# Optimization experiments

Measured on AMD Instinct MI355X. Metric: run time of the kernel, lower is better.

Reference implementation:

```python
import jax, jax.numpy as jnp
import numpy as np


def _maxpool2(x):
    # 2x2 max pool, stride 2; x: [B, C, H, W]
    B, C, H, W = x.shape
    return x.reshape(B, C, H // 2, 2, W // 2, 2).max(axis=(3, 5))


def setup_inputs() -> dict:
    key = jax.random.key(0)
    ks = jax.random.split(key, 6)
    B, C, H, W = 8, 256, 64, 64
    x = jax.random.normal(ks[0], (B, C, H, W), dtype=jnp.float32)
    w_theta = jax.random.normal(ks[1], (C // 8, C), dtype=jnp.float32) * (C ** -0.5)
    w_phi = jax.random.normal(ks[2], (C // 8, C), dtype=jnp.float32) * (C ** -0.5)
    w_g = jax.random.normal(ks[3], (C // 2, C), dtype=jnp.float32) * (C ** -0.5)
    w_o = jax.random.normal(ks[4], (C, C // 2), dtype=jnp.float32) * ((C // 2) ** -0.5)
    gamma = jnp.ones((), dtype=jnp.float32)
    return {"x": x, "w_theta": w_theta, "w_phi": w_phi, "w_g": w_g, "w_o": w_o, "gamma": gamma}


def reference(x, w_theta, w_phi, w_g, w_o, gamma):
    B, C, H, W = x.shape
    N = H * W
    # 1x1 convs are channel-mixing matmuls
    theta = jnp.einsum('oc,bchw->bohw', w_theta, x).reshape(B, C // 8, N)        # [B, C/8, N]
    phi = _maxpool2(jnp.einsum('oc,bchw->bohw', w_phi, x)).reshape(B, C // 8, N // 4)  # [B, C/8, N/4]
    g = _maxpool2(jnp.einsum('oc,bchw->bohw', w_g, x)).reshape(B, C // 2, N // 4)      # [B, C/2, N/4]
    # attention: softmax(theta^T phi) over pooled key axis
    beta = jax.nn.softmax(jnp.einsum('bcn,bcm->bnm', theta, phi), axis=-1)       # [B, N, N/4]
    o = jnp.einsum('bcm,bnm->bcn', g, beta).reshape(B, C // 2, H, W)             # [B, C/2, H, W]
    o = jnp.einsum('oc,bchw->bohw', w_o, o)                                      # [B, C, H, W]
    return gamma * o + x
```

## Files before the change

### kernel.cpp

```cpp
#include <hip/hip_runtime.h>

#define B_ 8
#define C_ 256
#define N_ 4096
#define CK 32
#define CG 128
#define M_ 1024

typedef __attribute__((ext_vector_type(8))) short bf16x8;
typedef __attribute__((ext_vector_type(4))) float f32x4;

__device__ __forceinline__ short f2bf(float f) {
  union { float f; unsigned u; } v; v.f = f;
  unsigned r = (v.u + 0x7FFF + ((v.u >> 16) & 1)) >> 16;
  return (short)r;
}
__device__ __forceinline__ int cvtpk(float lo, float hi) {
  int r;
  asm("v_cvt_pk_bf16_f32 %0, %1, %2" : "=v"(r) : "v"(lo), "v"(hi));
  return r;
}
__device__ __forceinline__ bf16x8 asbf(int4 v) {
  union { int4 i; bf16x8 b; } u; u.i = v; return u.b;
}

__global__ __launch_bounds__(512) void proj_kernel(const float* __restrict__ x,
                                                   const float* __restrict__ wt,
                                                   const float* __restrict__ wp,
                                                   const float* __restrict__ wg,
                                                   short* __restrict__ theta_t,
                                                   short* __restrict__ phi_t,
                                                   short* __restrict__ g_bf) {
  __shared__ __align__(16) short w_s[192 * 256];
  __shared__ __align__(16) short x_s[64 * 256];
  int tid = threadIdx.x;
  int bx = blockIdx.x, b = blockIdx.y;
  int t = bx >> 1, half = bx & 1;

#pragma unroll
  for (int rep = 0; rep < 12; ++rep) {
    int idx = rep * 512 + tid;
    int o = idx >> 5, gp = idx & 31;
    const float* src = (o < 32) ? (wt + o * 256)
                     : (o < 64) ? (wp + (o - 32) * 256)
                                : (wg + (o - 64) * 256);
    float4 f0 = *(const float4*)(src + gp * 8);
    float4 f1 = *(const float4*)(src + gp * 8 + 4);
    int4 pk;
    pk.x = cvtpk(f0.x, f0.y); pk.y = cvtpk(f0.z, f0.w);
    pk.z = cvtpk(f1.x, f1.y); pk.w = cvtpk(f1.z, f1.w);
    *(int4*)&w_s[o * 256 + ((gp ^ (o & 7)) * 8)] = pk;
  }
  {
    int l = tid & 63, cq = tid >> 6;
    int xoff = l >> 1, dy = l & 1;
    int n = t * 128 + dy * 64 + half * 32 + xoff;
    const float* xb = x + (size_t)b * C_ * N_ + n;
#pragma unroll
    for (int rep = 0; rep < 2; ++rep) {
      int ch = cq + rep * 8;
      int c0 = ch * 16;
      float f[16];
#pragma unroll
      for (int i = 0; i < 16; ++i) f[i] = xb[(size_t)(c0 + i) * N_];
      int4 pa, pb;
      pa.x = cvtpk(f[0], f[1]);   pa.y = cvtpk(f[2], f[3]);
      pa.z = cvtpk(f[4], f[5]);   pa.w = cvtpk(f[6], f[7]);
      pb.x = cvtpk(f[8], f[9]);   pb.y = cvtpk(f[10], f[11]);
      pb.z = cvtpk(f[12], f[13]); pb.w = cvtpk(f[14], f[15]);
      *(int4*)&x_s[l * 256 + (((2 * ch) ^ (l & 7)) * 8)] = pa;
      *(int4*)&x_s[l * 256 + (((2 * ch + 1) ^ (l & 7)) * 8)] = pb;
    }
  }
  __syncthreads();

  int lane = tid & 63, w = tid >> 6;
  int h = lane >> 4, q = lane & 15;
  int ns = w & 3, ow = w >> 2;
  f32x4 acc[6];
#pragma unroll
  for (int j = 0; j < 6; ++j) acc[j] = (f32x4){0.f, 0.f, 0.f, 0.f};

  int nl = 16 * ns + q;
#pragma unroll
  for (int ks = 0; ks < 8; ++ks) {
    bf16x8 bfr = *(const bf16x8*)&x_s[nl * 256 + (((4 * ks + h) ^ (nl & 7)) * 8)];
#pragma unroll
    for (int j = 0; j < 6; ++j) {
      int o = 16 * (6 * ow + j) + q;
      bf16x8 afr = *(const bf16x8*)&w_s[o * 256 + (((4 * ks + h) ^ (o & 7)) * 8)];
      acc[j] = __builtin_amdgcn_mfma_f32_16x16x32_bf16(afr, bfr, acc[j], 0, 0, 0);
    }
  }

  int xoff = nl >> 1, dy = nl & 1;
  int n = t * 128 + dy * 64 + half * 32 + xoff;
  int m = t * 32 + half * 16 + (nl >> 2);
#pragma unroll
  for (int j = 0; j < 6; ++j) {
    int ot = 6 * ow + j;
    if (ot < 2) {
      int2 pp;
      pp.x = cvtpk(acc[j][0], acc[j][1]);
      pp.y = cvtpk(acc[j][2], acc[j][3]);
      *(int2*)&theta_t[((size_t)b * N_ + n) * CK + ot * 16 + 4 * h] = pp;
    } else {
      float v[4];
#pragma unroll
      for (int r = 0; r < 4; ++r) {
        float vv = acc[j][r];
        vv = fmaxf(vv, __shfl_xor(vv, 1));
        vv = fmaxf(vv, __shfl_xor(vv, 2));
        v[r] = vv;
      }
      if ((nl & 3) == 0) {
        if (ot < 4) {
          int2 pp;
          pp.x = cvtpk(v[0], v[1]);
          pp.y = cvtpk(v[2], v[3]);
          *(int2*)&phi_t[((size_t)b * M_ + m) * CK + (ot - 2) * 16 + 4 * h] = pp;
        } else {
#pragma unroll
          for (int r = 0; r < 4; ++r) {
            int oc = (ot - 4) * 16 + 4 * h + r;
            g_bf[((size_t)b * CG + oc) * M_ + m] = f2bf(v[r]);
          }
        }
      }
    }
  }
}

__global__ __launch_bounds__(256, 3) void attn_out_kernel(const short* __restrict__ theta_t,
                                                          const short* __restrict__ phi_t,
                                                          const short* __restrict__ g_bf,
                                                          const float* __restrict__ wo,
                                                          const float* __restrict__ x,
                                                          const float* __restrict__ gamma,
                                                          float* __restrict__ out) {
  __shared__ __align__(16) short lds[25088];
  short* g_s = lds;
  short* p_sb = lds + 18432;

  int tid = threadIdx.x;
  int lane = tid & 63, w = tid >> 6;
  int h = lane >> 4, q = lane & 15;
  int bid = blockIdx.x;
  int b = bid & 7, n0 = (bid >> 3) * 64;
  int n = n0 + 16 * w + q;
  float gm = gamma[0];

  bf16x8 qfrag = *(const bf16x8*)&theta_t[((size_t)b * N_ + n) * CK + 8 * h];

  f32x4 Oacc[8];
#pragma unroll
  for (int ct = 0; ct < 8; ++ct) Oacc[ct] = (f32x4){0.f, 0.f, 0.f, 0.f};
  float S = 0.f;
  const f32x4 zero4 = {0.f, 0.f, 0.f, 0.f};

  int gm_ = tid & 7;
  short* p_sw = p_sb + w * 1152;
  const short* phi_b = phi_t + (size_t)b * M_ * CK;

  int4 pcur[4];
#pragma unroll
  for (int mt = 0; mt < 4; ++mt)
    pcur[mt] = *(const int4*)&phi_b[(16 * mt + q) * CK + 8 * h];
#pragma unroll
  for (int k = 0; k < 4; ++k) {
    int gc = (k * 256 + tid) >> 3;
    *(int4*)&g_s[gc * 72 + 8 * gm_] =
        *(const int4*)&g_bf[((size_t)b * CG + gc) * M_ + 8 * gm_];
  }
  __syncthreads();

  for (int it = 0; it < 16; ++it) {
    int cur = it & 1;
    const short* g_c = g_s + cur * 9216;
    int4 pnxt[4], rg[4];
    if (it < 15) {
      int m0n = (it + 1) * 64;
#pragma unroll
      for (int mt = 0; mt < 4; ++mt)
        pnxt[mt] = *(const int4*)&phi_b[(m0n + 16 * mt + q) * CK + 8 * h];
#pragma unroll
      for (int k = 0; k < 4; ++k) {
        int gc = (k * 256 + tid) >> 3;
        rg[k] = *(const int4*)&g_bf[((size_t)b * CG + gc) * M_ + m0n + 8 * gm_];
      }
    }

    f32x4 pt[4];
#pragma unroll
    for (int mt = 0; mt < 4; ++mt)
      pt[mt] = __builtin_amdgcn_mfma_f32_16x16x32_bf16(asbf(pcur[mt]), qfrag, zero4, 0, 0, 0);

#pragma unroll
    for (int mt = 0; mt < 4; ++mt) {
      float e0 = __expf(pt[mt][0]);
      float e1 = __expf(pt[mt][1]);
      float e2 = __expf(pt[mt][2]);
      float e3 = __expf(pt[mt][3]);
      S += (e0 + e1) + (e2 + e3);
      int2 pk;
      pk.x = cvtpk(e0, e1);
      pk.y = cvtpk(e2, e3);
      *(int2*)&p_sw[q * 72 + 16 * mt + 4 * h] = pk;
    }

    __builtin_amdgcn_s_setprio(1);
#pragma unroll
    for (int kp = 0; kp < 2; ++kp) {
      bf16x8 pf = *(const bf16x8*)&p_sw[q * 72 + 32 * kp + 8 * h];
#pragma unroll
      for (int ct = 0; ct < 8; ++ct) {
        bf16x8 vf = *(const bf16x8*)&g_c[(16 * ct + q) * 72 + 32 * kp + 8 * h];
        Oacc[ct] = __builtin_amdgcn_mfma_f32_16x16x32_bf16(vf, pf, Oacc[ct], 0, 0, 0);
      }
    }
    __builtin_amdgcn_s_setprio(0);

    if (it < 15) {
      int nxt = cur ^ 1;
#pragma unroll
      for (int k = 0; k < 4; ++k) {
        int gc = (k * 256 + tid) >> 3;
        *(int4*)&g_s[nxt * 9216 + gc * 72 + 8 * gm_] = rg[k];
      }
#pragma unroll
      for (int mt = 0; mt < 4; ++mt) pcur[mt] = pnxt[mt];
    }
    __syncthreads();
  }

  S += __shfl_xor(S, 16);
  S += __shfl_xor(S, 32);

  short* ot_s = lds;
  short* wo_s = lds + 8704;
  float rS = 1.f / S;
  int nloc = 16 * w + q;
#pragma unroll
  for (int ct = 0; ct < 8; ++ct) {
    int2 pp;
    pp.x = cvtpk(Oacc[ct][0] * rS, Oacc[ct][1] * rS);
    pp.y = cvtpk(Oacc[ct][2] * rS, Oacc[ct][3] * rS);
    *(int2*)&ot_s[nloc * 136 + 16 * ct + 4 * h] = pp;
  }

#pragma unroll
  for (int ho = 0; ho < 2; ++ho) {
#pragma unroll
    for (int rep = 0; rep < 8; ++rep) {
      int idx = rep * 256 + tid;
      int ol = idx >> 4, gp = idx & 15;
      const float* src = wo + (size_t)(128 * ho + ol) * 128 + gp * 8;
      float4 f0 = *(const float4*)src;
      float4 f1 = *(const float4*)(src + 4);
      int4 pk;
      pk.x = cvtpk(f0.x, f0.y); pk.y = cvtpk(f0.z, f0.w);
      pk.z = cvtpk(f1.x, f1.y); pk.w = cvtpk(f1.z, f1.w);
      *(int4*)&wo_s[ol * 128 + ((gp ^ (ol & 7)) * 8)] = pk;
    }
    __syncthreads();

    f32x4 acc[2][4];
#pragma unroll
    for (int j = 0; j < 2; ++j)
#pragma unroll
      for (int nt = 0; nt < 4; ++nt) acc[j][nt] = (f32x4){0.f, 0.f, 0.f, 0.f};

#pragma unroll
    for (int ks = 0; ks < 4; ++ks) {
      bf16x8 bfr[4];
#pragma unroll
      for (int nt = 0; nt < 4; ++nt)
        bfr[nt] = *(const bf16x8*)&ot_s[(16 * nt + q) * 136 + 32 * ks + 8 * h];
#pragma unroll
      for (int j = 0; j < 2; ++j) {
        int ol = 32 * w + 16 * j + q;
        bf16x8 afr = *(const bf16x8*)&wo_s[ol * 128 + (((4 * ks + h) ^ (ol & 7)) * 8)];
#pragma unroll
        for (int nt = 0; nt < 4; ++nt)
          acc[j][nt] = __builtin_amdgcn_mfma_f32_16x16x32_bf16(afr, bfr[nt], acc[j][nt], 0, 0, 0);
      }
    }

#pragma unroll
    for (int j = 0; j < 2; ++j)
#pragma unroll
      for (int nt = 0; nt < 4; ++nt)
#pragma unroll
        for (int r = 0; r < 4; ++r) {
          int o = 128 * ho + 32 * w + 16 * j + 4 * h + r;
          int nn = n0 + 16 * nt + q;
          size_t idx = ((size_t)b * C_ + o) * N_ + nn;
          out[idx] = gm * acc[j][nt][r] + x[idx];
        }
    if (ho == 0) __syncthreads();
  }
}

extern "C" void kernel_launch(void* const* d_in, const int* in_sizes, int n_in,
                              void* d_out, int out_size, void* d_ws, size_t ws_size,
                              hipStream_t stream) {
  const float* x = (const float*)d_in[0];
  const float* wt = (const float*)d_in[1];
  const float* wp = (const float*)d_in[2];
  const float* wg = (const float*)d_in[3];
  const float* wo = (const float*)d_in[4];
  const float* gamma = (const float*)d_in[5];
  float* out = (float*)d_out;

  short* theta_t = (short*)d_ws;
  short* phi_t = theta_t + (size_t)B_ * N_ * CK;
  short* g_bf = phi_t + (size_t)B_ * M_ * CK;

  proj_kernel<<<dim3(64, 8), 512, 0, stream>>>(x, wt, wp, wg, theta_t, phi_t, g_bf);
  attn_out_kernel<<<dim3(512), 256, 0, stream>>>(theta_t, phi_t, g_bf, wo, x, gamma, out);
}
```

Before: 56.49 us.

## Keep softmax probabilities in registers by permuting g layout; shrink attention blocks

The projection kernel now stores g with a permuted key index so that the packed exp values each lane already holds in its MFMA output line up with the B-operand layout of the PV MFMA. This drops the LDS round trip for the probability tile. The attention kernel also moves to 128-thread blocks covering 32 queries, giving 1024 blocks, with a reworked output-projection tiling. The trade-off is that each block now loads the full g and wo tiles for half as many queries, which doubles that reload traffic per query.

```diff
diff --git a/kernel.cpp b/kernel.cpp
--- a/kernel.cpp
+++ b/kernel.cpp
@@ -96,6 +96,7 @@
   int xoff = nl >> 1, dy = nl & 1;
   int n = t * 128 + dy * 64 + half * 32 + xoff;
   int m = t * 32 + half * 16 + (nl >> 2);
+  int mp = (m & ~31) | (((m >> 2) & 3) << 3) | (((m >> 4) & 1) << 2) | (m & 3);
 #pragma unroll
   for (int j = 0; j < 6; ++j) {
     int ot = 6 * ow + j;
@@ -123,7 +124,7 @@
 #pragma unroll
           for (int r = 0; r < 4; ++r) {
             int oc = (ot - 4) * 16 + 4 * h + r;
-            g_bf[((size_t)b * CG + oc) * M_ + m] = f2bf(v[r]);
+            g_bf[((size_t)b * CG + oc) * M_ + mp] = f2bf(v[r]);
           }
         }
       }
@@ -131,22 +132,21 @@
   }
 }
 
-__global__ __launch_bounds__(256, 3) void attn_out_kernel(const short* __restrict__ theta_t,
+__global__ __launch_bounds__(128, 2) void attn_out_kernel(const short* __restrict__ theta_t,
                                                           const short* __restrict__ phi_t,
                                                           const short* __restrict__ g_bf,
                                                           const float* __restrict__ wo,
                                                           const float* __restrict__ x,
                                                           const float* __restrict__ gamma,
                                                           float* __restrict__ out) {
-  __shared__ __align__(16) short lds[25088];
+  __shared__ __align__(16) short lds[18432];
   short* g_s = lds;
-  short* p_sb = lds + 18432;
 
   int tid = threadIdx.x;
   int lane = tid & 63, w = tid >> 6;
   int h = lane >> 4, q = lane & 15;
   int bid = blockIdx.x;
-  int b = bid & 7, n0 = (bid >> 3) * 64;
+  int b = bid & 7, n0 = (bid >> 3) * 32;
   int n = n0 + 16 * w + q;
   float gm = gamma[0];
 
@@ -158,35 +158,35 @@
   float S = 0.f;
   const f32x4 zero4 = {0.f, 0.f, 0.f, 0.f};
 
-  int gm_ = tid & 7;
-  short* p_sw = p_sb + w * 1152;
   const short* phi_b = phi_t + (size_t)b * M_ * CK;
+  const short* g_b = g_bf + (size_t)b * CG * M_;
 
   int4 pcur[4];
 #pragma unroll
   for (int mt = 0; mt < 4; ++mt)
     pcur[mt] = *(const int4*)&phi_b[(16 * mt + q) * CK + 8 * h];
 #pragma unroll
-  for (int k = 0; k < 4; ++k) {
-    int gc = (k * 256 + tid) >> 3;
-    *(int4*)&g_s[gc * 72 + 8 * gm_] =
-        *(const int4*)&g_bf[((size_t)b * CG + gc) * M_ + 8 * gm_];
+  for (int k = 0; k < 8; ++k) {
+    int idx = k * 128 + tid;
+    int gc = idx >> 3, gmm = idx & 7;
+    *(int4*)&g_s[gc * 72 + 8 * gmm] = *(const int4*)&g_b[(size_t)gc * M_ + 8 * gmm];
   }
   __syncthreads();
 
   for (int it = 0; it < 16; ++it) {
     int cur = it & 1;
     const short* g_c = g_s + cur * 9216;
-    int4 pnxt[4], rg[4];
+    int4 pnxt[4], rg[8];
     if (it < 15) {
       int m0n = (it + 1) * 64;
 #pragma unroll
       for (int mt = 0; mt < 4; ++mt)
         pnxt[mt] = *(const int4*)&phi_b[(m0n + 16 * mt + q) * CK + 8 * h];
 #pragma unroll
-      for (int k = 0; k < 4; ++k) {
-        int gc = (k * 256 + tid) >> 3;
-        rg[k] = *(const int4*)&g_bf[((size_t)b * CG + gc) * M_ + m0n + 8 * gm_];
+      for (int k = 0; k < 8; ++k) {
+        int idx = k * 128 + tid;
+        int gc = idx >> 3, gmm = idx & 7;
+        rg[k] = *(const int4*)&g_b[(size_t)gc * M_ + m0n + 8 * gmm];
       }
     }
 
@@ -195,6 +195,7 @@
     for (int mt = 0; mt < 4; ++mt)
       pt[mt] = __builtin_amdgcn_mfma_f32_16x16x32_bf16(asbf(pcur[mt]), qfrag, zero4, 0, 0, 0);
 
+    int2 pk[4];
 #pragma unroll
     for (int mt = 0; mt < 4; ++mt) {
       float e0 = __expf(pt[mt][0]);
@@ -202,16 +203,17 @@
       float e2 = __expf(pt[mt][2]);
       float e3 = __expf(pt[mt][3]);
       S += (e0 + e1) + (e2 + e3);
-      int2 pk;
-      pk.x = cvtpk(e0, e1);
-      pk.y = cvtpk(e2, e3);
-      *(int2*)&p_sw[q * 72 + 16 * mt + 4 * h] = pk;
+      pk[mt].x = cvtpk(e0, e1);
+      pk[mt].y = cvtpk(e2, e3);
     }
 
     __builtin_amdgcn_s_setprio(1);
 #pragma unroll
     for (int kp = 0; kp < 2; ++kp) {
-      bf16x8 pf = *(const bf16x8*)&p_sw[q * 72 + 32 * kp + 8 * h];
+      int4 pfi;
+      pfi.x = pk[2 * kp].x;     pfi.y = pk[2 * kp].y;
+      pfi.z = pk[2 * kp + 1].x; pfi.w = pk[2 * kp + 1].y;
+      bf16x8 pf = asbf(pfi);
 #pragma unroll
       for (int ct = 0; ct < 8; ++ct) {
         bf16x8 vf = *(const bf16x8*)&g_c[(16 * ct + q) * 72 + 32 * kp + 8 * h];
@@ -223,9 +225,10 @@
     if (it < 15) {
       int nxt = cur ^ 1;
 #pragma unroll
-      for (int k = 0; k < 4; ++k) {
-        int gc = (k * 256 + tid) >> 3;
-        *(int4*)&g_s[nxt * 9216 + gc * 72 + 8 * gm_] = rg[k];
+      for (int k = 0; k < 8; ++k) {
+        int idx = k * 128 + tid;
+        int gc = idx >> 3, gmm = idx & 7;
+        *(int4*)&g_s[nxt * 9216 + gc * 72 + 8 * gmm] = rg[k];
       }
 #pragma unroll
       for (int mt = 0; mt < 4; ++mt) pcur[mt] = pnxt[mt];
@@ -237,7 +240,7 @@
   S += __shfl_xor(S, 32);
 
   short* ot_s = lds;
-  short* wo_s = lds + 8704;
+  short* wo_s = lds + 4352;
   float rS = 1.f / S;
   int nloc = 16 * w + q;
 #pragma unroll
@@ -249,55 +252,45 @@
   }
 
 #pragma unroll
-  for (int ho = 0; ho < 2; ++ho) {
+  for (int tq = 0; tq < 4; ++tq) {
 #pragma unroll
     for (int rep = 0; rep < 8; ++rep) {
-      int idx = rep * 256 + tid;
+      int idx = rep * 128 + tid;
       int ol = idx >> 4, gp = idx & 15;
-      const float* src = wo + (size_t)(128 * ho + ol) * 128 + gp * 8;
+      const float* src = wo + (size_t)(64 * tq + ol) * 128 + gp * 8;
       float4 f0 = *(const float4*)src;
       float4 f1 = *(const float4*)(src + 4);
-      int4 pk;
-      pk.x = cvtpk(f0.x, f0.y); pk.y = cvtpk(f0.z, f0.w);
-      pk.z = cvtpk(f1.x, f1.y); pk.w = cvtpk(f1.z, f1.w);
-      *(int4*)&wo_s[ol * 128 + ((gp ^ (ol & 7)) * 8)] = pk;
+      int4 pk2;
+      pk2.x = cvtpk(f0.x, f0.y); pk2.y = cvtpk(f0.z, f0.w);
+      pk2.z = cvtpk(f1.x, f1.y); pk2.w = cvtpk(f1.z, f1.w);
+      *(int4*)&wo_s[ol * 128 + ((gp ^ (ol & 7)) * 8)] = pk2;
     }
     __syncthreads();
 
-    f32x4 acc[2][4];
-#pragma unroll
-    for (int j = 0; j < 2; ++j)
-#pragma unroll
-      for (int nt = 0; nt < 4; ++nt) acc[j][nt] = (f32x4){0.f, 0.f, 0.f, 0.f};
+    f32x4 acc[4];
+#pragma unroll
+    for (int j = 0; j < 4; ++j) acc[j] = (f32x4){0.f, 0.f, 0.f, 0.f};
 
 #pragma unroll
     for (int ks = 0; ks < 4; ++ks) {
-      bf16x8 bfr[4];
-#pragma unroll
-      for (int nt = 0; nt < 4; ++nt)
-        bfr[nt] = *(const bf16x8*)&ot_s[(16 * nt + q) * 136 + 32 * ks + 8 * h];
-#pragma unroll
-      for (int j = 0; j < 2; ++j) {
-        int ol = 32 * w + 16 * j + q;
+      bf16x8 bfr = *(const bf16x8*)&ot_s[(16 * w + q) * 136 + 32 * ks + 8 * h];
+#pragma unroll
+      for (int j = 0; j < 4; ++j) {
+        int ol = 16 * j + q;
         bf16x8 afr = *(const bf16x8*)&wo_s[ol * 128 + (((4 * ks + h) ^ (ol & 7)) * 8)];
-#pragma unroll
-        for (int nt = 0; nt < 4; ++nt)
-          acc[j][nt] = __builtin_amdgcn_mfma_f32_16x16x32_bf16(afr, bfr[nt], acc[j][nt], 0, 0, 0);
-      }
-    }
-
-#pragma unroll
-    for (int j = 0; j < 2; ++j)
-#pragma unroll
-      for (int nt = 0; nt < 4; ++nt)
-#pragma unroll
-        for (int r = 0; r < 4; ++r) {
-          int o = 128 * ho + 32 * w + 16 * j + 4 * h + r;
-          int nn = n0 + 16 * nt + q;
-          size_t idx = ((size_t)b * C_ + o) * N_ + nn;
-          out[idx] = gm * acc[j][nt][r] + x[idx];
-        }
-    if (ho == 0) __syncthreads();
+        acc[j] = __builtin_amdgcn_mfma_f32_16x16x32_bf16(afr, bfr, acc[j], 0, 0, 0);
+      }
+    }
+
+#pragma unroll
+    for (int j = 0; j < 4; ++j)
+#pragma unroll
+      for (int r = 0; r < 4; ++r) {
+        int o = 64 * tq + 16 * j + 4 * h + r;
+        size_t idx = ((size_t)b * C_ + o) * N_ + n;
+        out[idx] = gm * acc[j][r] + x[idx];
+      }
+    __syncthreads();
   }
 }
 
@@ -317,5 +310,5 @@
   short* g_bf = phi_t + (size_t)B_ * M_ * CK;
 
   proj_kernel<<<dim3(64, 8), 512, 0, stream>>>(x, wt, wp, wg, theta_t, phi_t, g_bf);
-  attn_out_kernel<<<dim3(512), 256, 0, stream>>>(theta_t, phi_t, g_bf, wo, x, gamma, out);
-}
+  attn_out_kernel<<<dim3(1024), 128, 0, stream>>>(theta_t, phi_t, g_bf, wo, x, gamma, out);
+}
```

New measurement: 53.93 us. 4.5% less time.

## Permute g storage to feed MFMA directly from registers, skip P LDS round-trip

Applied to the files above, without the earlier changes.

The projection kernel now writes g with a permuted key index, so the softmax probabilities produced by the first MFMA can be used directly as the B operand of the second MFMA without passing through LDS. Each wave loads its g fragments straight from global memory into registers instead of staging them cooperatively through double-buffered LDS, which removes the per-iteration __syncthreads. theta weights are prescaled by log2(e) so a raw v_exp_f32 replaces __expf. The costs are much higher register pressure (launch bounds lowered from 3 to 2 blocks per SM) and redundant global/L2 reads of g across the four waves.

```diff
diff --git a/kernel.cpp b/kernel.cpp
--- a/kernel.cpp
+++ b/kernel.cpp
@@ -18,6 +18,11 @@
 __device__ __forceinline__ int cvtpk(float lo, float hi) {
   int r;
   asm("v_cvt_pk_bf16_f32 %0, %1, %2" : "=v"(r) : "v"(lo), "v"(hi));
+  return r;
+}
+__device__ __forceinline__ float vexp2(float x) {
+  float r;
+  asm("v_exp_f32 %0, %1" : "=v"(r) : "v"(x));
   return r;
 }
 __device__ __forceinline__ bf16x8 asbf(int4 v) {
@@ -44,11 +49,12 @@
     const float* src = (o < 32) ? (wt + o * 256)
                      : (o < 64) ? (wp + (o - 32) * 256)
                                 : (wg + (o - 64) * 256);
+    float sc = (o < 32) ? 1.44269504f : 1.f;
     float4 f0 = *(const float4*)(src + gp * 8);
     float4 f1 = *(const float4*)(src + gp * 8 + 4);
     int4 pk;
-    pk.x = cvtpk(f0.x, f0.y); pk.y = cvtpk(f0.z, f0.w);
-    pk.z = cvtpk(f1.x, f1.y); pk.w = cvtpk(f1.z, f1.w);
+    pk.x = cvtpk(f0.x * sc, f0.y * sc); pk.y = cvtpk(f0.z * sc, f0.w * sc);
+    pk.z = cvtpk(f1.x * sc, f1.y * sc); pk.w = cvtpk(f1.z * sc, f1.w * sc);
     *(int4*)&w_s[o * 256 + ((gp ^ (o & 7)) * 8)] = pk;
   }
   {
@@ -96,6 +102,7 @@
   int xoff = nl >> 1, dy = nl & 1;
   int n = t * 128 + dy * 64 + half * 32 + xoff;
   int m = t * 32 + half * 16 + (nl >> 2);
+  int mp = (m & ~31) | (((m >> 2) & 3) << 3) | (((m >> 4) & 1) << 2) | (m & 3);
 #pragma unroll
   for (int j = 0; j < 6; ++j) {
     int ot = 6 * ow + j;
@@ -123,7 +130,7 @@
 #pragma unroll
           for (int r = 0; r < 4; ++r) {
             int oc = (ot - 4) * 16 + 4 * h + r;
-            g_bf[((size_t)b * CG + oc) * M_ + m] = f2bf(v[r]);
+            g_bf[((size_t)b * CG + oc) * M_ + mp] = f2bf(v[r]);
           }
         }
       }
@@ -131,7 +138,7 @@
   }
 }
 
-__global__ __launch_bounds__(256, 3) void attn_out_kernel(const short* __restrict__ theta_t,
+__global__ __launch_bounds__(256, 2) void attn_out_kernel(const short* __restrict__ theta_t,
                                                           const short* __restrict__ phi_t,
                                                           const short* __restrict__ g_bf,
                                                           const float* __restrict__ wo,
@@ -139,8 +146,6 @@
                                                           const float* __restrict__ gamma,
                                                           float* __restrict__ out) {
   __shared__ __align__(16) short lds[25088];
-  short* g_s = lds;
-  short* p_sb = lds + 18432;
 
   int tid = threadIdx.x;
   int lane = tid & 63, w = tid >> 6;
@@ -158,36 +163,28 @@
   float S = 0.f;
   const f32x4 zero4 = {0.f, 0.f, 0.f, 0.f};
 
-  int gm_ = tid & 7;
-  short* p_sw = p_sb + w * 1152;
   const short* phi_b = phi_t + (size_t)b * M_ * CK;
+  const short* g_b = g_bf + (size_t)b * CG * M_;
 
   int4 pcur[4];
 #pragma unroll
   for (int mt = 0; mt < 4; ++mt)
     pcur[mt] = *(const int4*)&phi_b[(16 * mt + q) * CK + 8 * h];
-#pragma unroll
-  for (int k = 0; k < 4; ++k) {
-    int gc = (k * 256 + tid) >> 3;
-    *(int4*)&g_s[gc * 72 + 8 * gm_] =
-        *(const int4*)&g_bf[((size_t)b * CG + gc) * M_ + 8 * gm_];
-  }
-  __syncthreads();
 
   for (int it = 0; it < 16; ++it) {
-    int cur = it & 1;
-    const short* g_c = g_s + cur * 9216;
-    int4 pnxt[4], rg[4];
+    int m0 = it * 64;
+    int4 vf[16];
+#pragma unroll
+    for (int ct = 0; ct < 8; ++ct)
+#pragma unroll
+      for (int kp = 0; kp < 2; ++kp)
+        vf[2 * ct + kp] =
+            *(const int4*)&g_b[(size_t)(16 * ct + q) * M_ + m0 + 32 * kp + 8 * h];
+    int4 pnxt[4];
     if (it < 15) {
-      int m0n = (it + 1) * 64;
 #pragma unroll
       for (int mt = 0; mt < 4; ++mt)
-        pnxt[mt] = *(const int4*)&phi_b[(m0n + 16 * mt + q) * CK + 8 * h];
-#pragma unroll
-      for (int k = 0; k < 4; ++k) {
-        int gc = (k * 256 + tid) >> 3;
-        rg[k] = *(const int4*)&g_bf[((size_t)b * CG + gc) * M_ + m0n + 8 * gm_];
-      }
+        pnxt[mt] = *(const int4*)&phi_b[(m0 + 64 + 16 * mt + q) * CK + 8 * h];
     }
 
     f32x4 pt[4];
@@ -195,42 +192,36 @@
     for (int mt = 0; mt < 4; ++mt)
       pt[mt] = __builtin_amdgcn_mfma_f32_16x16x32_bf16(asbf(pcur[mt]), qfrag, zero4, 0, 0, 0);
 
+    int2 pk[4];
 #pragma unroll
     for (int mt = 0; mt < 4; ++mt) {
-      float e0 = __expf(pt[mt][0]);
-      float e1 = __expf(pt[mt][1]);
-      float e2 = __expf(pt[mt][2]);
-      float e3 = __expf(pt[mt][3]);
+      float e0 = vexp2(pt[mt][0]);
+      float e1 = vexp2(pt[mt][1]);
+      float e2 = vexp2(pt[mt][2]);
+      float e3 = vexp2(pt[mt][3]);
       S += (e0 + e1) + (e2 + e3);
-      int2 pk;
-      pk.x = cvtpk(e0, e1);
-      pk.y = cvtpk(e2, e3);
-      *(int2*)&p_sw[q * 72 + 16 * mt + 4 * h] = pk;
+      pk[mt].x = cvtpk(e0, e1);
+      pk[mt].y = cvtpk(e2, e3);
     }
 
     __builtin_amdgcn_s_setprio(1);
 #pragma unroll
     for (int kp = 0; kp < 2; ++kp) {
-      bf16x8 pf = *(const bf16x8*)&p_sw[q * 72 + 32 * kp + 8 * h];
-#pragma unroll
-      for (int ct = 0; ct < 8; ++ct) {
-        bf16x8 vf = *(const bf16x8*)&g_c[(16 * ct + q) * 72 + 32 * kp + 8 * h];
-        Oacc[ct] = __builtin_amdgcn_mfma_f32_16x16x32_bf16(vf, pf, Oacc[ct], 0, 0, 0);
-      }
+      int4 pfi;
+      pfi.x = pk[2 * kp].x;     pfi.y = pk[2 * kp].y;
+      pfi.z = pk[2 * kp + 1].x; pfi.w = pk[2 * kp + 1].y;
+      bf16x8 pf = asbf(pfi);
+#pragma unroll
+      for (int ct = 0; ct < 8; ++ct)
+        Oacc[ct] = __builtin_amdgcn_mfma_f32_16x16x32_bf16(asbf(vf[2 * ct + kp]), pf,
+                                                           Oacc[ct], 0, 0, 0);
     }
     __builtin_amdgcn_s_setprio(0);
 
     if (it < 15) {
-      int nxt = cur ^ 1;
-#pragma unroll
-      for (int k = 0; k < 4; ++k) {
-        int gc = (k * 256 + tid) >> 3;
-        *(int4*)&g_s[nxt * 9216 + gc * 72 + 8 * gm_] = rg[k];
-      }
 #pragma unroll
       for (int mt = 0; mt < 4; ++mt) pcur[mt] = pnxt[mt];
     }
-    __syncthreads();
   }
 
   S += __shfl_xor(S, 16);
@@ -257,10 +248,10 @@
       const float* src = wo + (size_t)(128 * ho + ol) * 128 + gp * 8;
       float4 f0 = *(const float4*)src;
       float4 f1 = *(const float4*)(src + 4);
-      int4 pk;
-      pk.x = cvtpk(f0.x, f0.y); pk.y = cvtpk(f0.z, f0.w);
-      pk.z = cvtpk(f1.x, f1.y); pk.w = cvtpk(f1.z, f1.w);
-      *(int4*)&wo_s[ol * 128 + ((gp ^ (ol & 7)) * 8)] = pk;
+      int4 pk2;
+      pk2.x = cvtpk(f0.x, f0.y); pk2.y = cvtpk(f0.z, f0.w);
+      pk2.z = cvtpk(f1.x, f1.y); pk2.w = cvtpk(f1.z, f1.w);
+      *(int4*)&wo_s[ol * 128 + ((gp ^ (ol & 7)) * 8)] = pk2;
     }
     __syncthreads();
 
```

Measured after the change: 97.31 us. 1.72x slower.
